# Kernel tuning notes

Hardware: AMD Instinct MI355X
Metric: run time of the kernel (lower is better)

The kernel has to match this reference:

```python
import jax, jax.numpy as jnp
import numpy as np

HEADS = 4
DIM_HEAD = 32
DIM = 128
HIDDEN = HEADS * DIM_HEAD  # 128
LN_EPS = 1e-6


def setup_inputs() -> dict:
    key = jax.random.key(0)
    ks = jax.random.split(key, 4)
    b, X, Y, Z = 4, 32, 32, 32
    x = jax.random.normal(ks[0], (b, X, Y, Z, DIM), dtype=jnp.float32)
    # 1x1x1 convs are pointwise linears: kernel [in, out]
    w_qkv = jax.random.normal(ks[1], (DIM, 3 * HIDDEN), dtype=jnp.float32) * (DIM ** -0.5)
    w_out = jax.random.normal(ks[2], (HIDDEN, DIM), dtype=jnp.float32) * (HIDDEN ** -0.5)
    b_out = jax.random.normal(ks[3], (DIM,), dtype=jnp.float32) * 0.02
    ln_scale = jnp.ones((DIM,), dtype=jnp.float32)
    ln_bias = jnp.zeros((DIM,), dtype=jnp.float32)
    return {"x": x, "w_qkv": w_qkv, "w_out": w_out, "b_out": b_out,
            "ln_scale": ln_scale, "ln_bias": ln_bias}


def reference(x, w_qkv, w_out, b_out, ln_scale, ln_bias):
    b, X, Y, Z, c = x.shape
    n = X * Y * Z
    scale = DIM_HEAD ** (-0.5)

    # 1x1x1 conv (no bias) == pointwise matmul over channels
    qkv = jnp.einsum('bxyzc,cd->bxyzd', x, w_qkv)  # [b,X,Y,Z,3*hidden]
    q, k, v = jnp.split(qkv, 3, axis=-1)

    # rearrange 'b x y z (h c) -> b h c n'
    def to_bhcn(t):
        return t.reshape(b, n, HEADS, DIM_HEAD).transpose(0, 2, 3, 1)

    q, k, v = to_bhcn(q), to_bhcn(k), to_bhcn(v)

    q = jax.nn.softmax(q, axis=-2) * scale   # softmax over feature dim d
    k = jax.nn.softmax(k, axis=-1)           # softmax over token dim n

    context = jnp.einsum('bhdn,bhcn->bhdc', k, v)   # [b,h,d,c] small d=c=32
    out = jnp.einsum('bhde,bhdn->bhen', context, q) # [b,h,e,n]

    # rearrange 'b h c n -> b x y z (h c)' (cubic volume, matching original)
    out = out.transpose(0, 3, 1, 2).reshape(b, X, Y, Z, HIDDEN)

    # final 1x1x1 conv with bias
    out = jnp.einsum('bxyzh,hc->bxyzc', out, w_out) + b_out

    # LayerNorm over last axis (flax default eps=1e-6, with scale+bias)
    mu = jnp.mean(out, axis=-1, keepdims=True)
    var = jnp.mean(jnp.square(out - mu), axis=-1, keepdims=True)
    out = (out - mu) * jax.lax.rsqrt(var + LN_EPS) * ln_scale + ln_bias
    return out
```

## Files before the change

### kernel.cpp

```cpp
#include <hip/hip_runtime.h>
#include <hip/hip_bf16.h>

typedef _Float16 f16;
typedef _Float16 f16x4 __attribute__((ext_vector_type(4)));
typedef _Float16 f16x8 __attribute__((ext_vector_type(8)));
typedef float f32x4 __attribute__((ext_vector_type(4)));

#define MFMA(a, b, c) __builtin_amdgcn_mfma_f32_16x16x32_f16((a), (b), (c), 0, 0, 0)

#define BB 4
#define NPOS 32768
#define HH 4
#define NBLK 1024
#define NBLK3 4096
#define STATB 2304
#define LDP 136

__device__ __forceinline__ f16x8 ldx8(const float* p) {
  float4 a = *(const float4*)p;
  float4 b = *(const float4*)(p + 4);
  return (f16x8){(f16)a.x, (f16)a.y, (f16)a.z, (f16)a.w,
                 (f16)b.x, (f16)b.y, (f16)b.z, (f16)b.w};
}

__global__ __launch_bounds__(256)
void la_k0_prep(const float* __restrict__ wqkv, f16* __restrict__ wkvF,
                f16* __restrict__ wqF) {
  const int g0 = blockIdx.x * 256 + threadIdx.x;
  for (int i = g0; i < 32768; i += 16384) {
    int j = i & 7, l = (i >> 3) & 63, ks = (i >> 9) & 3, nt = (i >> 11) & 3,
        h = i >> 13;
    int n = 16 * nt + (l & 15);
    int c = 32 * ks + 8 * (l >> 4) + j;
    int col = (n < 32) ? (128 + h * 32 + n) : (256 + h * 32 + (n - 32));
    wkvF[i] = (f16)wqkv[c * 384 + col];
  }
  {
    int i = g0;
    int j = i & 7, l = (i >> 3) & 63, ks = (i >> 9) & 3, a = (i >> 11) & 1,
        h = i >> 12;
    int row = l & 15;
    int n = 8 * (row >> 2) + 4 * a + (row & 3);
    int c = 32 * ks + 8 * (l >> 4) + j;
    wqF[i] = (f16)wqkv[c * 384 + h * 32 + n];
  }
}

__global__ __launch_bounds__(256, 4)
void la_k1_stats(const float* __restrict__ x, const f16* __restrict__ wkvF,
                 const f16* __restrict__ wqF, char* __restrict__ stats,
                 f16* __restrict__ Qhat) {
  const int blk = blockIdx.x, t = threadIdx.x;
  const int w = t >> 6, l = t & 63, lg = l >> 4, ln = l & 15;

  __shared__ __align__(16) f16 EV[2][64 * LDP];

  const float* xb = x + (size_t)blk * (128 * 128);
  f16x8 xf[2][4];
#pragma unroll
  for (int mi = 0; mi < 2; ++mi)
#pragma unroll
    for (int ks = 0; ks < 4; ++ks)
      xf[mi][ks] = ldx8(xb + (32 * w + 16 * mi + ln) * 128 + 32 * ks + 8 * lg);

  const f32x4 Z4 = {0.f, 0.f, 0.f, 0.f};

  auto logits = [&](int h, f32x4 (&acc)[2][4]) {
#pragma unroll
    for (int mi = 0; mi < 2; ++mi)
#pragma unroll
      for (int nt = 0; nt < 4; ++nt) acc[mi][nt] = Z4;
#pragma unroll
    for (int ks = 0; ks < 4; ++ks) {
#pragma unroll
      for (int nt = 0; nt < 4; ++nt) {
        f16x8 bf = *(const f16x8*)(wkvF + (((h * 4 + nt) * 4 + ks) << 9) + l * 8);
        acc[0][nt] = MFMA(xf[0][ks], bf, acc[0][nt]);
        acc[1][nt] = MFMA(xf[1][ks], bf, acc[1][nt]);
      }
    }
  };

  auto qlog = [&](int h, f32x4 (&qa)[2][2]) {
#pragma unroll
    for (int mi = 0; mi < 2; ++mi)
#pragma unroll
      for (int a = 0; a < 2; ++a) qa[mi][a] = Z4;
#pragma unroll
    for (int ks = 0; ks < 4; ++ks) {
      f16x8 a0 = *(const f16x8*)(wqF + (((h * 2 + 0) * 4 + ks) << 9) + l * 8);
      f16x8 a1 = *(const f16x8*)(wqF + (((h * 2 + 1) * 4 + ks) << 9) + l * 8);
#pragma unroll
      for (int mi = 0; mi < 2; ++mi) {
        qa[mi][0] = MFMA(a0, xf[mi][ks], qa[mi][0]);
        qa[mi][1] = MFMA(a1, xf[mi][ks], qa[mi][1]);
      }
    }
  };

  auto qfin = [&](int h, f32x4 (&qa)[2][2]) {
#pragma unroll
    for (int mi = 0; mi < 2; ++mi) {
      float s = 0.f;
#pragma unroll
      for (int a = 0; a < 2; ++a)
#pragma unroll
        for (int r = 0; r < 4; ++r) {
          qa[mi][a][r] = __expf(qa[mi][a][r]);
          s += qa[mi][a][r];
        }
      s += __shfl_xor(s, 16);
      s += __shfl_xor(s, 32);
      const float inv = 0.17677669529663688f / s;
      f16x8 af = (f16x8){(f16)(qa[mi][0][0] * inv), (f16)(qa[mi][0][1] * inv),
                         (f16)(qa[mi][0][2] * inv), (f16)(qa[mi][0][3] * inv),
                         (f16)(qa[mi][1][0] * inv), (f16)(qa[mi][1][1] * inv),
                         (f16)(qa[mi][1][2] * inv), (f16)(qa[mi][1][3] * inv)};
      f16* qp = Qhat + (((size_t)(blk * 8 + 2 * w + mi) * 4 + h) << 9) + l * 8;
      *(f16x8*)qp = af;
    }
  };

  auto phaseA = [&](int h, f32x4 (&acc)[2][4]) {
    f16* E = (f16*)EV[h & 1];
    float sl[2] = {0.f, 0.f};
#pragma unroll
    for (int nt = 0; nt < 2; ++nt)
#pragma unroll
      for (int mi = 0; mi < 2; ++mi) {
        float e0 = __expf(acc[mi][nt][0]);
        float e1 = __expf(acc[mi][nt][1]);
        float e2 = __expf(acc[mi][nt][2]);
        float e3 = __expf(acc[mi][nt][3]);
        sl[nt] += (e0 + e1) + (e2 + e3);
        *(f16x4*)&E[(16 * nt + ln) * LDP + 32 * w + 16 * mi + 4 * lg] =
            (f16x4){(f16)e0, (f16)e1, (f16)e2, (f16)e3};
        f32x4 vv = acc[mi][nt + 2];
        *(f16x4*)&E[(32 + 16 * nt + ln) * LDP + 32 * w + 16 * mi + 4 * lg] =
            (f16x4){(f16)vv[0], (f16)vv[1], (f16)vv[2], (f16)vv[3]};
      }
#pragma unroll
    for (int nt = 0; nt < 2; ++nt) {
      sl[nt] += __shfl_xor(sl[nt], 16);
      sl[nt] += __shfl_xor(sl[nt], 32);
    }
    f16* sp = (f16*)(stats + (size_t)(blk * HH + h) * STATB + 2048);
    if (lg == 0) {
      sp[ln * 4 + w] = (f16)sl[0];
      sp[(16 + ln) * 4 + w] = (f16)sl[1];
    }
  };

  auto phaseB = [&](int h) {
    __syncthreads();
    const f16* E = (const f16*)EV[h & 1];
    const int tm = w >> 1, tn = w & 1;
    f32x4 tacc = Z4;
#pragma unroll
    for (int ks = 0; ks < 4; ++ks) {
      f16x8 ea = *(const f16x8*)&E[(16 * tm + ln) * LDP + 32 * ks + 8 * lg];
      f16x8 vb = *(const f16x8*)&E[(32 + 16 * tn + ln) * LDP + 32 * ks + 8 * lg];
      tacc = MFMA(ea, vb, tacc);
    }
    f16* tp = (f16*)(stats + (size_t)(blk * HH + h) * STATB);
#pragma unroll
    for (int r = 0; r < 4; ++r)
      tp[(16 * tm + 4 * lg + r) * 32 + 16 * tn + ln] = (f16)tacc[r];
  };

  f32x4 accA[2][4], accB[2][4], qa[2][2];
  logits(0, accA);
  phaseA(0, accA); qlog(0, qa); qfin(0, qa); logits(1, accB); phaseB(0);
  phaseA(1, accB); qlog(1, qa); qfin(1, qa); logits(2, accA); phaseB(1);
  phaseA(2, accA); qlog(2, qa); qfin(2, qa); logits(3, accB); phaseB(2);
  phaseA(3, accB); qlog(3, qa); qfin(3, qa); phaseB(3);
}

__global__ __launch_bounds__(256)
void la_k2_combine(const char* __restrict__ stats, f16* __restrict__ ctxN) {
  const int gid = blockIdx.x;
  const int bh = gid >> 5, d = gid & 31;
  const int b = bh >> 2, h = bh & 3;
  const int t = threadIdx.x, w = t >> 6, l = t & 63;
  const int c = t & 31, grp = t >> 5;
  __shared__ float redt[4][32];
  __shared__ float reds[4];

  float sg = 0.f, tc = 0.f;
  for (int i = grp; i < 256; i += 8) {
    const char* ub = stats + (size_t)((b * 256 + i) * HH + h) * STATB;
    tc += (float)((const f16*)ub)[d * 32 + c];
    f16x4 s4 = *(const f16x4*)(ub + 2048 + d * 8);
    sg += ((float)s4[0] + (float)s4[1]) + ((float)s4[2] + (float)s4[3]);
  }
  tc += __shfl_xor(tc, 32);
  sg += __shfl_xor(sg, 32);
  if (l < 32) redt[w][l] = tc;
  if (l == 0) reds[w] = sg;
  __syncthreads();
  if (t < 32) {
    float tt = (redt[0][t] + redt[1][t]) + (redt[2][t] + redt[3][t]);
    float ss = (reds[0] + reds[1]) + (reds[2] + reds[3]);
    ctxN[((size_t)bh * 32 + d) * 32 + t] = (f16)(tt / ss);
  }
}

__global__ __launch_bounds__(256)
void la_k2b_fold(const f16* __restrict__ ctxN, const float* __restrict__ wout,
                 f16* __restrict__ GTF) {
  const int b = blockIdx.x, t = threadIdx.x;
  const int h = t >> 6, l = t & 63, lg = l >> 4, ln = l & 15;
  const f32x4 Z4 = {0.f, 0.f, 0.f, 0.f};

  const f16* cb = ctxN + (size_t)((b * HH + h) * 32) * 32;
  f16x8 bfrag[2];
#pragma unroll
  for (int nt = 0; nt < 2; ++nt)
    bfrag[nt] = *(const f16x8*)(cb + (16 * nt + ln) * 32 + 8 * lg);

  f16* gf = GTF + (size_t)b * 16384;
#pragma unroll
  for (int mt = 0; mt < 8; ++mt) {
    f16x8 af;
#pragma unroll
    for (int j = 0; j < 8; ++j)
      af[j] = (f16)wout[(32 * h + 8 * lg + j) * 128 + 16 * mt + ln];
#pragma unroll
    for (int nt = 0; nt < 2; ++nt) {
      f32x4 acc = MFMA(af, bfrag[nt], Z4);
#pragma unroll
      for (int r = 0; r < 4; ++r) {
        int dsub = 16 * nt + ln;
        gf[((h * 8 + mt) << 9) + (16 * (dsub >> 3) + 4 * lg + r) * 8 + (dsub & 7)] =
            (f16)acc[r];
      }
    }
  }
}

__global__ __launch_bounds__(64)
void la_k3_out(const f16* __restrict__ Qhat, const f16* __restrict__ GTF,
               const float* __restrict__ bout, const float* __restrict__ lns,
               const float* __restrict__ lnb, float* __restrict__ out) {
  const int blk = blockIdx.x;
  const int l = threadIdx.x, lg = l >> 4, ln = l & 15;
  const int b = blk >> 10;

  const f32x4 Z4 = {0.f, 0.f, 0.f, 0.f};
  const f16* gf = GTF + (size_t)b * 16384;

  f16x8 af[2][4];
#pragma unroll
  for (int g = 0; g < 2; ++g)
#pragma unroll
    for (int h = 0; h < HH; ++h)
      af[g][h] = *(const f16x8*)(Qhat +
          (((size_t)(blk * 2 + g) * 4 + h) << 9) + l * 8);

  f32x4 y[2][8];
#pragma unroll
  for (int g = 0; g < 2; ++g)
#pragma unroll
    for (int nc = 0; nc < 8; ++nc) y[g][nc] = Z4;

#pragma unroll
  for (int h = 0; h < HH; ++h) {
#pragma unroll
    for (int nc = 0; nc < 8; ++nc) {
      f16x8 gfr = *(const f16x8*)(gf + (((h * 8 + nc) << 9) + l * 8));
      y[0][nc] = MFMA(gfr, af[0][h], y[0][nc]);
      y[1][nc] = MFMA(gfr, af[1][h], y[1][nc]);
    }
  }

#pragma unroll
  for (int nc = 0; nc < 8; ++nc) {
    f32x4 bb = *(const f32x4*)(bout + 16 * nc + 4 * lg);
    y[0][nc] += bb;
    y[1][nc] += bb;
  }

#pragma unroll
  for (int g = 0; g < 2; ++g) {
    float s = 0.f;
#pragma unroll
    for (int nc = 0; nc < 8; ++nc)
      s += (y[g][nc][0] + y[g][nc][1]) + (y[g][nc][2] + y[g][nc][3]);
    s += __shfl_xor(s, 16);
    s += __shfl_xor(s, 32);
    const float mean = s * (1.f / 128.f);
    float v = 0.f;
#pragma unroll
    for (int nc = 0; nc < 8; ++nc)
#pragma unroll
      for (int r = 0; r < 4; ++r) {
        float dv = y[g][nc][r] - mean;
        v = fmaf(dv, dv, v);
      }
    v += __shfl_xor(v, 16);
    v += __shfl_xor(v, 32);
    const float inv = rsqrtf(v * (1.f / 128.f) + 1e-6f);

    float* op = out + (size_t)(blk * 32 + 16 * g + ln) * 128;
#pragma unroll
    for (int nc = 0; nc < 8; ++nc) {
      f32x4 sv = *(const f32x4*)(lns + 16 * nc + 4 * lg);
      f32x4 b2 = *(const f32x4*)(lnb + 16 * nc + 4 * lg);
      f32x4 o4;
#pragma unroll
      for (int r = 0; r < 4; ++r)
        o4[r] = (y[g][nc][r] - mean) * inv * sv[r] + b2[r];
      *(f32x4*)(op + 16 * nc + 4 * lg) = o4;
    }
  }
}

extern "C" void kernel_launch(void* const* d_in, const int* in_sizes, int n_in,
                              void* d_out, int out_size, void* d_ws, size_t ws_size,
                              hipStream_t stream) {
  const float* x = (const float*)d_in[0];
  const float* w_qkv = (const float*)d_in[1];
  const float* w_out = (const float*)d_in[2];
  const float* b_out = (const float*)d_in[3];
  const float* ln_s = (const float*)d_in[4];
  const float* ln_b = (const float*)d_in[5];
  float* out = (float*)d_out;

  char* ws = (char*)d_ws;
  char* stats = ws;
  f16* wkvF = (f16*)(ws + 9437184);
  f16* wqF = (f16*)(ws + 9437184 + 65536);
  f16* GTF = (f16*)(ws + 9437184 + 65536 + 32768);
  f16* ctxN = (f16*)(ws + 9437184 + 65536 + 32768 + 131072);
  f16* Qhat = (f16*)(ws + 9437184 + 65536 + 32768 + 131072 + 32768);

  la_k0_prep<<<dim3(64), 256, 0, stream>>>(w_qkv, wkvF, wqF);
  la_k1_stats<<<dim3(NBLK), 256, 0, stream>>>(x, wkvF, wqF, stats, Qhat);
  la_k2_combine<<<dim3(512), 256, 0, stream>>>(stats, ctxN);
  la_k2b_fold<<<dim3(BB), 256, 0, stream>>>(ctxN, w_out, GTF);
  la_k3_out<<<dim3(NBLK3), 64, 0, stream>>>(Qhat, GTF, b_out, ln_s, ln_b, out);
}
```

Baseline: 77.58 us.

## Serialize per-head loop in stats kernel to cut registers and LDS for occupancy

Replaces the software-pipelined, double-buffered per-head schedule in the stats kernel with a plain rolled loop over heads that uses a single LDS buffer and two barriers per head. The launch bound rises from 4 to 8 blocks per CU, so the compiler has to fit the kernel in fewer registers and can keep more waves resident. The cost is that logits for the next head no longer overlap with the current head's E·V product, and there is an extra barrier per head.

```diff
diff --git a/kernel.cpp b/kernel.cpp
--- a/kernel.cpp
+++ b/kernel.cpp
@@ -46,14 +46,14 @@
   }
 }
 
-__global__ __launch_bounds__(256, 4)
+__global__ __launch_bounds__(256, 8)
 void la_k1_stats(const float* __restrict__ x, const f16* __restrict__ wkvF,
                  const f16* __restrict__ wqF, char* __restrict__ stats,
                  f16* __restrict__ Qhat) {
   const int blk = blockIdx.x, t = threadIdx.x;
   const int w = t >> 6, l = t & 63, lg = l >> 4, ln = l & 15;
 
-  __shared__ __align__(16) f16 EV[2][64 * LDP];
+  __shared__ __align__(16) f16 EV[64 * LDP];
 
   const float* xb = x + (size_t)blk * (128 * 128);
   f16x8 xf[2][4];
@@ -65,7 +65,9 @@
 
   const f32x4 Z4 = {0.f, 0.f, 0.f, 0.f};
 
-  auto logits = [&](int h, f32x4 (&acc)[2][4]) {
+#pragma unroll 1
+  for (int h = 0; h < HH; ++h) {
+    f32x4 acc[2][4];
 #pragma unroll
     for (int mi = 0; mi < 2; ++mi)
 #pragma unroll
@@ -79,101 +81,93 @@
         acc[1][nt] = MFMA(xf[1][ks], bf, acc[1][nt]);
       }
     }
-  };
-
-  auto qlog = [&](int h, f32x4 (&qa)[2][2]) {
-#pragma unroll
-    for (int mi = 0; mi < 2; ++mi)
-#pragma unroll
-      for (int a = 0; a < 2; ++a) qa[mi][a] = Z4;
-#pragma unroll
-    for (int ks = 0; ks < 4; ++ks) {
-      f16x8 a0 = *(const f16x8*)(wqF + (((h * 2 + 0) * 4 + ks) << 9) + l * 8);
-      f16x8 a1 = *(const f16x8*)(wqF + (((h * 2 + 1) * 4 + ks) << 9) + l * 8);
+
+    {
+      float sl[2] = {0.f, 0.f};
+#pragma unroll
+      for (int nt = 0; nt < 2; ++nt)
+#pragma unroll
+        for (int mi = 0; mi < 2; ++mi) {
+          float e0 = __expf(acc[mi][nt][0]);
+          float e1 = __expf(acc[mi][nt][1]);
+          float e2 = __expf(acc[mi][nt][2]);
+          float e3 = __expf(acc[mi][nt][3]);
+          sl[nt] += (e0 + e1) + (e2 + e3);
+          *(f16x4*)&EV[(16 * nt + ln) * LDP + 32 * w + 16 * mi + 4 * lg] =
+              (f16x4){(f16)e0, (f16)e1, (f16)e2, (f16)e3};
+          f32x4 vv = acc[mi][nt + 2];
+          *(f16x4*)&EV[(32 + 16 * nt + ln) * LDP + 32 * w + 16 * mi + 4 * lg] =
+              (f16x4){(f16)vv[0], (f16)vv[1], (f16)vv[2], (f16)vv[3]};
+        }
+#pragma unroll
+      for (int nt = 0; nt < 2; ++nt) {
+        sl[nt] += __shfl_xor(sl[nt], 16);
+        sl[nt] += __shfl_xor(sl[nt], 32);
+      }
+      f16* sp = (f16*)(stats + (size_t)(blk * HH + h) * STATB + 2048);
+      if (lg == 0) {
+        sp[ln * 4 + w] = (f16)sl[0];
+        sp[(16 + ln) * 4 + w] = (f16)sl[1];
+      }
+    }
+
+    __syncthreads();
+
+    {
+      const int tm = w >> 1, tn = w & 1;
+      f32x4 tacc = Z4;
+#pragma unroll
+      for (int ks = 0; ks < 4; ++ks) {
+        f16x8 ea = *(const f16x8*)&EV[(16 * tm + ln) * LDP + 32 * ks + 8 * lg];
+        f16x8 vb = *(const f16x8*)&EV[(32 + 16 * tn + ln) * LDP + 32 * ks + 8 * lg];
+        tacc = MFMA(ea, vb, tacc);
+      }
+      f16* tp = (f16*)(stats + (size_t)(blk * HH + h) * STATB);
+#pragma unroll
+      for (int r = 0; r < 4; ++r)
+        tp[(16 * tm + 4 * lg + r) * 32 + 16 * tn + ln] = (f16)tacc[r];
+    }
+
+    {
+      f32x4 qa[2][2];
+#pragma unroll
+      for (int mi = 0; mi < 2; ++mi)
+#pragma unroll
+        for (int a = 0; a < 2; ++a) qa[mi][a] = Z4;
+#pragma unroll
+      for (int ks = 0; ks < 4; ++ks) {
+        f16x8 a0 = *(const f16x8*)(wqF + (((h * 2 + 0) * 4 + ks) << 9) + l * 8);
+        f16x8 a1 = *(const f16x8*)(wqF + (((h * 2 + 1) * 4 + ks) << 9) + l * 8);
+#pragma unroll
+        for (int mi = 0; mi < 2; ++mi) {
+          qa[mi][0] = MFMA(a0, xf[mi][ks], qa[mi][0]);
+          qa[mi][1] = MFMA(a1, xf[mi][ks], qa[mi][1]);
+        }
+      }
 #pragma unroll
       for (int mi = 0; mi < 2; ++mi) {
-        qa[mi][0] = MFMA(a0, xf[mi][ks], qa[mi][0]);
-        qa[mi][1] = MFMA(a1, xf[mi][ks], qa[mi][1]);
-      }
-    }
-  };
-
-  auto qfin = [&](int h, f32x4 (&qa)[2][2]) {
-#pragma unroll
-    for (int mi = 0; mi < 2; ++mi) {
-      float s = 0.f;
-#pragma unroll
-      for (int a = 0; a < 2; ++a)
-#pragma unroll
-        for (int r = 0; r < 4; ++r) {
-          qa[mi][a][r] = __expf(qa[mi][a][r]);
-          s += qa[mi][a][r];
-        }
-      s += __shfl_xor(s, 16);
-      s += __shfl_xor(s, 32);
-      const float inv = 0.17677669529663688f / s;
-      f16x8 af = (f16x8){(f16)(qa[mi][0][0] * inv), (f16)(qa[mi][0][1] * inv),
-                         (f16)(qa[mi][0][2] * inv), (f16)(qa[mi][0][3] * inv),
-                         (f16)(qa[mi][1][0] * inv), (f16)(qa[mi][1][1] * inv),
-                         (f16)(qa[mi][1][2] * inv), (f16)(qa[mi][1][3] * inv)};
-      f16* qp = Qhat + (((size_t)(blk * 8 + 2 * w + mi) * 4 + h) << 9) + l * 8;
-      *(f16x8*)qp = af;
-    }
-  };
-
-  auto phaseA = [&](int h, f32x4 (&acc)[2][4]) {
-    f16* E = (f16*)EV[h & 1];
-    float sl[2] = {0.f, 0.f};
-#pragma unroll
-    for (int nt = 0; nt < 2; ++nt)
-#pragma unroll
-      for (int mi = 0; mi < 2; ++mi) {
-        float e0 = __expf(acc[mi][nt][0]);
-        float e1 = __expf(acc[mi][nt][1]);
-        float e2 = __expf(acc[mi][nt][2]);
-        float e3 = __expf(acc[mi][nt][3]);
-        sl[nt] += (e0 + e1) + (e2 + e3);
-        *(f16x4*)&E[(16 * nt + ln) * LDP + 32 * w + 16 * mi + 4 * lg] =
-            (f16x4){(f16)e0, (f16)e1, (f16)e2, (f16)e3};
-        f32x4 vv = acc[mi][nt + 2];
-        *(f16x4*)&E[(32 + 16 * nt + ln) * LDP + 32 * w + 16 * mi + 4 * lg] =
-            (f16x4){(f16)vv[0], (f16)vv[1], (f16)vv[2], (f16)vv[3]};
-      }
-#pragma unroll
-    for (int nt = 0; nt < 2; ++nt) {
-      sl[nt] += __shfl_xor(sl[nt], 16);
-      sl[nt] += __shfl_xor(sl[nt], 32);
-    }
-    f16* sp = (f16*)(stats + (size_t)(blk * HH + h) * STATB + 2048);
-    if (lg == 0) {
-      sp[ln * 4 + w] = (f16)sl[0];
-      sp[(16 + ln) * 4 + w] = (f16)sl[1];
-    }
-  };
-
-  auto phaseB = [&](int h) {
+        float s = 0.f;
+#pragma unroll
+        for (int a = 0; a < 2; ++a)
+#pragma unroll
+          for (int r = 0; r < 4; ++r) {
+            qa[mi][a][r] = __expf(qa[mi][a][r]);
+            s += qa[mi][a][r];
+          }
+        s += __shfl_xor(s, 16);
+        s += __shfl_xor(s, 32);
+        const float inv = 0.17677669529663688f / s;
+        f16x8 af = (f16x8){(f16)(qa[mi][0][0] * inv), (f16)(qa[mi][0][1] * inv),
+                           (f16)(qa[mi][0][2] * inv), (f16)(qa[mi][0][3] * inv),
+                           (f16)(qa[mi][1][0] * inv), (f16)(qa[mi][1][1] * inv),
+                           (f16)(qa[mi][1][2] * inv), (f16)(qa[mi][1][3] * inv)};
+        f16* qp = Qhat + (((size_t)(blk * 8 + 2 * w + mi) * 4 + h) << 9) + l * 8;
+        *(f16x8*)qp = af;
+      }
+    }
+
     __syncthreads();
-    const f16* E = (const f16*)EV[h & 1];
-    const int tm = w >> 1, tn = w & 1;
-    f32x4 tacc = Z4;
-#pragma unroll
-    for (int ks = 0; ks < 4; ++ks) {
-      f16x8 ea = *(const f16x8*)&E[(16 * tm + ln) * LDP + 32 * ks + 8 * lg];
-      f16x8 vb = *(const f16x8*)&E[(32 + 16 * tn + ln) * LDP + 32 * ks + 8 * lg];
-      tacc = MFMA(ea, vb, tacc);
-    }
-    f16* tp = (f16*)(stats + (size_t)(blk * HH + h) * STATB);
-#pragma unroll
-    for (int r = 0; r < 4; ++r)
-      tp[(16 * tm + 4 * lg + r) * 32 + 16 * tn + ln] = (f16)tacc[r];
-  };
-
-  f32x4 accA[2][4], accB[2][4], qa[2][2];
-  logits(0, accA);
-  phaseA(0, accA); qlog(0, qa); qfin(0, qa); logits(1, accB); phaseB(0);
-  phaseA(1, accB); qlog(1, qa); qfin(1, qa); logits(2, accA); phaseB(1);
-  phaseA(2, accA); qlog(2, qa); qfin(2, qa); logits(3, accB); phaseB(2);
-  phaseA(3, accB); qlog(3, qa); qfin(3, qa); phaseB(3);
+  }
 }
 
 __global__ __launch_bounds__(256)
```

Result: slower. 122.3 us (+57.7%).
